# Optimization experiments

Hardware: AMD Instinct MI355X
Metric: run time of the kernel (lower is better)

## Reference

```python
import jax, jax.numpy as jnp
import numpy as np

B, C, N = 4, 3, 8192

def setup_inputs() -> dict:
    key = jax.random.key(0)
    k1, k2, k3 = jax.random.split(key, 3)
    return {
        "registration_pred": jax.random.normal(k1, (B, C, N), dtype=jnp.float32),
        "registration_gt": jax.random.normal(k2, (B, C, N), dtype=jnp.float32),
        "coords": jax.random.normal(k3, (B, C, N), dtype=jnp.float32),
    }

def reference(registration_pred, registration_gt, coords):
    # point clouds: [B, N, 3]
    pc1 = jnp.transpose(coords + registration_gt, (0, 2, 1))   # gt cloud
    pc2 = jnp.transpose(coords + registration_pred, (0, 2, 1)) # generated cloud
    sq1 = jnp.sum(pc1 * pc1, axis=-1)  # [B, N]
    sq2 = jnp.sum(pc2 * pc2, axis=-1)  # [B, M]
    dist = (-2.0 * jnp.einsum('bnc,bmc->bnm', pc1, pc2)
            + sq1[:, :, None] + sq2[:, None, :])
    dist1 = jnp.min(dist, axis=-1)  # nearest gen point for each gt point [B, N]
    dist2 = jnp.min(dist, axis=1)   # nearest gt point for each gen point [B, M]
    return jnp.mean(jnp.sum(dist1, axis=1)) + jnp.mean(jnp.sum(dist2, axis=1))
```

## Files before the change

### kernel.cpp

```cpp
#include <hip/hip_runtime.h>
#include <cfloat>
#include <cstdint>

#define BB    4
#define NN    8192
#define NT    8
#define TPB   256
#define NTILE (NT*TPB)
#define NBQ   (NN/NTILE)
#define MSL   64
#define MS    (NN/MSL)
#define NPAIR (MSL/2)
#define NHW   (TPB/32)

static __device__ __forceinline__ float vmin3(float a, float b, float c) {
    float r;
    asm("v_min3_f32 %0, %1, %2, %3" : "=v"(r) : "v"(a), "v"(b), "v"(c));
    return r;
}
static __device__ __forceinline__ float vmin2(float a, float b) {
    float r;
    asm("v_min_f32 %0, %1, %2" : "=v"(r) : "v"(a), "v"(b));
    return r;
}

__device__ __forceinline__ unsigned mapf(float f) {
    unsigned b = __float_as_uint(f);
    return b ^ ((unsigned)((int)b >> 31) | 0x80000000u);
}
__device__ __forceinline__ float unmapf(unsigned u) {
    unsigned b = u ^ (((u & 0x80000000u) != 0u) ? 0x80000000u : 0xFFFFFFFFu);
    return __uint_as_float(b);
}

__global__ __launch_bounds__(TPB) void chamfer_onepass_kernel(
    const float* __restrict__ pred, const float* __restrict__ gt,
    const float* __restrict__ coords, unsigned* __restrict__ ws)
{
    const int b  = blockIdx.y;
    const int nb = blockIdx.x & (NBQ - 1);
    const int ms = blockIdx.x >> 2;
    const size_t base = (size_t)b * 3 * NN;
    const float* gr = gt     + base;
    const float* pr = pred   + base;
    const float* cc = coords + base;

    __shared__ float4 tileE[NPAIR];
    __shared__ float4 tileO[NPAIR];
    __shared__ float  colmin[NHW][MSL];

    const int tid = threadIdx.x;

    if (tid < MSL) {
        int m   = ms * MSL + tid;
        float x = cc[m]        + pr[m];
        float y = cc[NN + m]   + pr[NN + m];
        float z = cc[2*NN + m] + pr[2*NN + m];
        float4 v = make_float4(-2.f*x, -2.f*y, -2.f*z, fmaf(x, x, fmaf(y, y, z*z)));
        if (tid & 1) tileO[tid >> 1] = v; else tileE[tid >> 1] = v;
    }
    #pragma unroll
    for (int j = tid; j < NHW * MSL; j += TPB) (&colmin[0][0])[j] = FLT_MAX;

    float px[NT], py[NT], pz[NT], sqn[NT], mv[NT];
    const int n0 = nb * NTILE + tid;
    #pragma unroll
    for (int k = 0; k < NT; ++k) {
        int n   = n0 + k * TPB;
        float x = cc[n]        + gr[n];
        float y = cc[NN + n]   + gr[NN + n];
        float z = cc[2*NN + n] + gr[2*NN + n];
        px[k] = x; py[k] = y; pz[k] = z;
        sqn[k] = fmaf(x, x, fmaf(y, y, z*z));
        mv[k]  = FLT_MAX;
    }
    __syncthreads();

    const int ll = tid & 31;
    float* cm = colmin[tid >> 5];

    int jp = ll;
    float4 a = tileE[jp];
    float4 c = tileO[jp];
    #pragma unroll 2
    for (int i = 0; i < NPAIR; ++i) {
        const int jn = (jp + 1) & (NPAIR - 1);
        float4 an = tileE[jn];
        float4 cn = tileO[jn];
        float d0[NT], d1[NT];
        #pragma unroll
        for (int k = 0; k < NT; ++k) {
            float w0 = a.w + sqn[k];
            float w1 = c.w + sqn[k];
            d0[k] = fmaf(px[k], a.x, fmaf(py[k], a.y, fmaf(pz[k], a.z, w0)));
            d1[k] = fmaf(px[k], c.x, fmaf(py[k], c.y, fmaf(pz[k], c.z, w1)));
            mv[k] = vmin3(mv[k], d0[k], d1[k]);
        }
        float t0 = vmin3(d0[0], d0[1], d0[2]);
        float u0 = vmin3(d0[3], d0[4], d0[5]);
        float s0 = vmin3(d0[6], d0[7], t0);
        float c0 = vmin2(s0, u0);
        float t1 = vmin3(d1[0], d1[1], d1[2]);
        float u1 = vmin3(d1[3], d1[4], d1[5]);
        float s1 = vmin3(d1[6], d1[7], t1);
        float c1 = vmin2(s1, u1);
        float2* slot = (float2*)&cm[2 * jp];
        float2 old = *slot;
        old.x = vmin2(old.x, c0);
        old.y = vmin2(old.y, c1);
        *slot = old;
        jp = jn; a = an; c = cn;
    }

    unsigned* wsrow = ws + (size_t)b * NN;
    #pragma unroll
    for (int k = 0; k < NT; ++k)
        atomicMin(&wsrow[n0 + k * TPB], mapf(mv[k]));

    __syncthreads();
    unsigned* wscol = ws + (size_t)BB * NN + (size_t)b * NN;
    if (tid < MSL) {
        float v = vmin3(colmin[0][tid], colmin[1][tid], colmin[2][tid]);
        v = vmin3(v, colmin[3][tid], colmin[4][tid]);
        v = vmin3(v, colmin[5][tid], colmin[6][tid]);
        v = vmin2(v, colmin[7][tid]);
        atomicMin(&wscol[ms * MSL + tid], mapf(v));
    }
}

__global__ __launch_bounds__(256) void ws_init_kernel(unsigned* __restrict__ ws)
{
    ((uint4*)ws)[blockIdx.x * 256 + threadIdx.x] = make_uint4(~0u, ~0u, ~0u, ~0u);
}

__global__ __launch_bounds__(256) void chamfer_reduce_a(
    const unsigned* __restrict__ ws, float* __restrict__ partial)
{
    int idx = blockIdx.x * 256 + threadIdx.x;
    const uint4* p = (const uint4*)ws;
    uint4 u = p[idx];
    float s = (unmapf(u.x) + unmapf(u.y)) + (unmapf(u.z) + unmapf(u.w));
    #pragma unroll
    for (int off = 32; off > 0; off >>= 1)
        s += __shfl_down(s, off);
    __shared__ float sm[4];
    if ((threadIdx.x & 63) == 0) sm[threadIdx.x >> 6] = s;
    __syncthreads();
    if (threadIdx.x == 0)
        partial[blockIdx.x] = (sm[0] + sm[1]) + (sm[2] + sm[3]);
}

__global__ __launch_bounds__(64) void chamfer_reduce_b(
    const float* __restrict__ partial, float* __restrict__ out)
{
    float s = partial[threadIdx.x];
    #pragma unroll
    for (int off = 32; off > 0; off >>= 1)
        s += __shfl_down(s, off);
    if (threadIdx.x == 0) out[0] = s * (1.0f / (float)BB);
}

extern "C" void kernel_launch(void* const* d_in, const int* in_sizes, int n_in,
                              void* d_out, int out_size, void* d_ws, size_t ws_size,
                              hipStream_t stream) {
    const float* pred   = (const float*)d_in[0];
    const float* gt     = (const float*)d_in[1];
    const float* coords = (const float*)d_in[2];
    unsigned*    wsu    = (unsigned*)d_ws;
    float*       part   = (float*)((char*)d_ws + (size_t)2 * BB * NN * sizeof(unsigned));
    float*       out    = (float*)d_out;

    ws_init_kernel<<<64, 256, 0, stream>>>(wsu);
    dim3 grid(NBQ * MS, BB);
    chamfer_onepass_kernel<<<grid, TPB, 0, stream>>>(pred, gt, coords, wsu);
    chamfer_reduce_a<<<64, 256, 0, stream>>>(wsu, part);
    chamfer_reduce_b<<<1, 64, 0, stream>>>(part, out);
}
```

Baseline: 43.63 us.

## Loop each block over four column slices with double-buffered shared tiles

Each block now walks four consecutive 64-point column slices instead of one. The next slice's global loads are issued before the current slice's compute and written to a second shared buffer afterwards. This cuts the grid by four, so the row-point loads and the per-row atomicMin traffic are amortized over more columns. In exchange it adds two barriers per slice, lowers block-level parallelism (512 blocks), and sets launch_bounds with a minimum of two blocks per SIMD/CU.

```diff
diff --git a/kernel.cpp b/kernel.cpp
--- a/kernel.cpp
+++ b/kernel.cpp
@@ -9,7 +9,8 @@
 #define NTILE (NT*TPB)
 #define NBQ   (NN/NTILE)
 #define MSL   64
-#define MS    (NN/MSL)
+#define LPB   4
+#define NCG   (NN/(MSL*LPB))
 #define NPAIR (MSL/2)
 #define NHW   (TPB/32)
 
@@ -33,33 +34,33 @@
     return __uint_as_float(b);
 }
 
-__global__ __launch_bounds__(TPB) void chamfer_onepass_kernel(
+__global__ __launch_bounds__(TPB, 2) void chamfer_onepass_kernel(
     const float* __restrict__ pred, const float* __restrict__ gt,
     const float* __restrict__ coords, unsigned* __restrict__ ws)
 {
     const int b  = blockIdx.y;
     const int nb = blockIdx.x & (NBQ - 1);
-    const int ms = blockIdx.x >> 2;
+    const int cg = blockIdx.x >> 2;
     const size_t base = (size_t)b * 3 * NN;
     const float* gr = gt     + base;
     const float* pr = pred   + base;
     const float* cc = coords + base;
 
-    __shared__ float4 tileE[NPAIR];
-    __shared__ float4 tileO[NPAIR];
+    __shared__ float4 tileE[2][NPAIR];
+    __shared__ float4 tileO[2][NPAIR];
     __shared__ float  colmin[NHW][MSL];
 
     const int tid = threadIdx.x;
+    const int colbase = cg * (LPB * MSL);
 
     if (tid < MSL) {
-        int m   = ms * MSL + tid;
+        int m   = colbase + tid;
         float x = cc[m]        + pr[m];
         float y = cc[NN + m]   + pr[NN + m];
         float z = cc[2*NN + m] + pr[2*NN + m];
         float4 v = make_float4(-2.f*x, -2.f*y, -2.f*z, fmaf(x, x, fmaf(y, y, z*z)));
-        if (tid & 1) tileO[tid >> 1] = v; else tileE[tid >> 1] = v;
+        if (tid & 1) tileO[0][tid >> 1] = v; else tileE[0][tid >> 1] = v;
     }
-    #pragma unroll
     for (int j = tid; j < NHW * MSL; j += TPB) (&colmin[0][0])[j] = FLT_MAX;
 
     float px[NT], py[NT], pz[NT], sqn[NT], mv[NT];
@@ -78,54 +79,80 @@
 
     const int ll = tid & 31;
     float* cm = colmin[tid >> 5];
-
-    int jp = ll;
-    float4 a = tileE[jp];
-    float4 c = tileO[jp];
-    #pragma unroll 2
-    for (int i = 0; i < NPAIR; ++i) {
-        const int jn = (jp + 1) & (NPAIR - 1);
-        float4 an = tileE[jn];
-        float4 cn = tileO[jn];
-        float d0[NT], d1[NT];
-        #pragma unroll
-        for (int k = 0; k < NT; ++k) {
-            float w0 = a.w + sqn[k];
-            float w1 = c.w + sqn[k];
-            d0[k] = fmaf(px[k], a.x, fmaf(py[k], a.y, fmaf(pz[k], a.z, w0)));
-            d1[k] = fmaf(px[k], c.x, fmaf(py[k], c.y, fmaf(pz[k], c.z, w1)));
-            mv[k] = vmin3(mv[k], d0[k], d1[k]);
-        }
-        float t0 = vmin3(d0[0], d0[1], d0[2]);
-        float u0 = vmin3(d0[3], d0[4], d0[5]);
-        float s0 = vmin3(d0[6], d0[7], t0);
-        float c0 = vmin2(s0, u0);
-        float t1 = vmin3(d1[0], d1[1], d1[2]);
-        float u1 = vmin3(d1[3], d1[4], d1[5]);
-        float s1 = vmin3(d1[6], d1[7], t1);
-        float c1 = vmin2(s1, u1);
-        float2* slot = (float2*)&cm[2 * jp];
-        float2 old = *slot;
-        old.x = vmin2(old.x, c0);
-        old.y = vmin2(old.y, c1);
-        *slot = old;
-        jp = jn; a = an; c = cn;
+    unsigned* wscol = ws + (size_t)BB * NN + (size_t)b * NN;
+
+    int cur = 0;
+    #pragma unroll 1
+    for (int s = 0; s < LPB; ++s) {
+        float r0, r1, r2, r3, r4, r5;
+        const bool do_stage = (tid < MSL) && (s + 1 < LPB);
+        if (do_stage) {
+            int m = colbase + (s + 1) * MSL + tid;
+            r0 = cc[m]; r1 = cc[NN + m]; r2 = cc[2*NN + m];
+            r3 = pr[m]; r4 = pr[NN + m]; r5 = pr[2*NN + m];
+        }
+
+        int jp = ll;
+        float4 a = tileE[cur][jp];
+        float4 c = tileO[cur][jp];
+        #pragma unroll 2
+        for (int i = 0; i < NPAIR; ++i) {
+            const int jn = (jp + 1) & (NPAIR - 1);
+            float4 an = tileE[cur][jn];
+            float4 cn = tileO[cur][jn];
+            float d0[NT], d1[NT];
+            #pragma unroll
+            for (int k = 0; k < NT; ++k) {
+                float w0 = a.w + sqn[k];
+                float w1 = c.w + sqn[k];
+                d0[k] = fmaf(px[k], a.x, fmaf(py[k], a.y, fmaf(pz[k], a.z, w0)));
+                d1[k] = fmaf(px[k], c.x, fmaf(py[k], c.y, fmaf(pz[k], c.z, w1)));
+                mv[k] = vmin3(mv[k], d0[k], d1[k]);
+            }
+            float t0 = vmin3(d0[0], d0[1], d0[2]);
+            float u0 = vmin3(d0[3], d0[4], d0[5]);
+            float s0 = vmin3(d0[6], d0[7], t0);
+            float c0 = vmin2(s0, u0);
+            float t1 = vmin3(d1[0], d1[1], d1[2]);
+            float u1 = vmin3(d1[3], d1[4], d1[5]);
+            float s1 = vmin3(d1[6], d1[7], t1);
+            float c1 = vmin2(s1, u1);
+            float2* slot = (float2*)&cm[2 * jp];
+            float2 old = *slot;
+            old.x = vmin2(old.x, c0);
+            old.y = vmin2(old.y, c1);
+            *slot = old;
+            jp = jn; a = an; c = cn;
+        }
+
+        if (do_stage) {
+            float x = r0 + r3, y = r1 + r4, z = r2 + r5;
+            float4 v = make_float4(-2.f*x, -2.f*y, -2.f*z,
+                                   fmaf(x, x, fmaf(y, y, z*z)));
+            if (tid & 1) tileO[cur ^ 1][tid >> 1] = v;
+            else         tileE[cur ^ 1][tid >> 1] = v;
+        }
+        __syncthreads();
+
+        if (tid < MSL) {
+            float v = vmin3(colmin[0][tid], colmin[1][tid], colmin[2][tid]);
+            v = vmin3(v, colmin[3][tid], colmin[4][tid]);
+            v = vmin3(v, colmin[5][tid], colmin[6][tid]);
+            v = vmin2(v, colmin[7][tid]);
+            atomicMin(&wscol[colbase + s * MSL + tid], mapf(v));
+        }
+        if (s + 1 < LPB) {
+            for (int j = tid; j < NHW * MSL; j += TPB)
+                (&colmin[0][0])[j] = FLT_MAX;
+        }
+        __syncthreads();
+        cur ^= 1;
     }
 
     unsigned* wsrow = ws + (size_t)b * NN;
     #pragma unroll
     for (int k = 0; k < NT; ++k)
         atomicMin(&wsrow[n0 + k * TPB], mapf(mv[k]));
-
-    __syncthreads();
-    unsigned* wscol = ws + (size_t)BB * NN + (size_t)b * NN;
-    if (tid < MSL) {
-        float v = vmin3(colmin[0][tid], colmin[1][tid], colmin[2][tid]);
-        v = vmin3(v, colmin[3][tid], colmin[4][tid]);
-        v = vmin3(v, colmin[5][tid], colmin[6][tid]);
-        v = vmin2(v, colmin[7][tid]);
-        atomicMin(&wscol[ms * MSL + tid], mapf(v));
-    }
 }
 
 __global__ __launch_bounds__(256) void ws_init_kernel(unsigned* __restrict__ ws)
@@ -171,7 +198,7 @@
     float*       out    = (float*)d_out;
 
     ws_init_kernel<<<64, 256, 0, stream>>>(wsu);
-    dim3 grid(NBQ * MS, BB);
+    dim3 grid(NBQ * NCG, BB);
     chamfer_onepass_kernel<<<grid, TPB, 0, stream>>>(pred, gt, coords, wsu);
     chamfer_reduce_a<<<64, 256, 0, stream>>>(wsu, part);
     chamfer_reduce_b<<<1, 64, 0, stream>>>(part, out);
```

New measurement: 48.96 us. 1.12x slower.
